# Performance work log

Hardware: AMD Instinct MI355X
Metric: run time of the kernel (lower is better)

Reference implementation:

```python
import jax, jax.numpy as jnp
import numpy as np

THRESHOLD = 0.5

def setup_inputs() -> dict:
    key = jax.random.key(0)
    k1, k2 = jax.random.split(key)
    N, F, B = 800000, 64, 8
    xs = jax.random.uniform(k1, (N, 1), dtype=jnp.float32)          # scores in [0,1)
    pl = jax.random.normal(k2, (N, F), dtype=jnp.float32)           # payload features
    rs = (jnp.arange(B + 1, dtype=jnp.int32) * (N // B))            # row splits [0,100k,...,800k]
    return {"xs": xs, "pl": pl, "rs": rs}

def reference(xs, pl, rs):
    # SelectThreshold(xs, pl, rs, threshold=0.5):
    #   keep rows with score > threshold, compact features, recompute row splits,
    #   and emit scatter indices (original row ids of the kept rows).
    # JIT-static variant: kept rows are stably compacted to the front of an
    # [N, F] buffer; slots >= n_sel are zero-padded, scatter idx padded with N.
    N = pl.shape[0]
    B = rs.shape[0] - 1
    mask = xs[:, 0] > THRESHOLD                                      # [N] bool
    # stable argsort: selected rows first, original (per-segment) order preserved
    order = jnp.argsort(jnp.logical_not(mask))                       # [N] int
    n_sel = jnp.sum(mask.astype(jnp.int32))
    valid = jnp.arange(N) < n_sel                                    # [N] bool
    newfeat = jnp.where(valid[:, None], pl[order], jnp.zeros((), pl.dtype))  # [N, F]
    scatter_idxs = jnp.where(valid, order, N).astype(jnp.int32)[:, None]     # [N, 1]
    # per-event selected counts -> new row splits
    seg_ids = jnp.searchsorted(rs, jnp.arange(N, dtype=rs.dtype), side='right') - 1  # [N]
    counts = jax.ops.segment_sum(mask.astype(rs.dtype), seg_ids, num_segments=B)     # [B]
    new_rs = jnp.concatenate([jnp.zeros((1,), rs.dtype), jnp.cumsum(counts)])        # [B+1]
    return newfeat, new_rs, scatter_idxs
```

## Files before the change

kernel.cpp:

```cpp
#include <hip/hip_runtime.h>


#define THRESH 0.5f
#define RPB 1024

__global__ void k_count(const float* __restrict__ xs, int N,
                        unsigned long long* __restrict__ bitmap,
                        int* __restrict__ blk_counts) {
    __shared__ int wc[16];
    const int tid  = threadIdx.x;
    const int lane = tid & 63, wave = tid >> 6;
    const int base = blockIdx.x * RPB;
    for (int c = 0; c < 4; ++c) {
        int i = base + c * 256 + tid;
        int m = (i < N) && (xs[i] > THRESH);
        unsigned long long bal = __ballot(m);
        if (lane == 0) {
            int rowstart = base + c * 256 + wave * 64;
            if (rowstart < N) bitmap[rowstart >> 6] = bal;
            wc[c * 4 + wave] = __popcll(bal);
        }
    }
    __syncthreads();
    if (tid == 0) {
        int s = 0;
        for (int k = 0; k < 16; ++k) s += wc[k];
        blk_counts[blockIdx.x] = s;
    }
}

__global__ void k_scan(const int* __restrict__ blk_counts, int nblocks,
                       const unsigned long long* __restrict__ bitmap,
                       const int* __restrict__ rs, int nrs, int N,
                       int* __restrict__ blk_off, int* __restrict__ nsel_out,
                       float* __restrict__ out_rs) {
    __shared__ int s[1024];
    const int t = threadIdx.x;
    int v = (t < nblocks) ? blk_counts[t] : 0;
    s[t] = v;
    __syncthreads();
    for (int d = 1; d < 1024; d <<= 1) {
        int add = (t >= d) ? s[t - d] : 0;
        __syncthreads();
        s[t] += add;
        __syncthreads();
    }
    int n_sel = s[1023];
    if (t < nblocks) blk_off[t] = s[t] - v;
    if (t == 0) nsel_out[0] = n_sel;
    if (t < nrs) {
        int j = rs[t];
        int val;
        if (j >= N)      val = n_sel;
        else if (j <= 0) val = 0;
        else {
            int blk = j >> 10;
            int cnt = (blk == 0) ? 0 : s[blk - 1];
            for (int w = (blk << 10) >> 6; w < (j >> 6); ++w)
                cnt += __popcll(bitmap[w]);
            int rem = j & 63;
            if (rem) cnt += __popcll(bitmap[j >> 6] & ((1ull << rem) - 1ull));
            val = cnt;
        }
        out_rs[t] = (float)val;
    }
}

__global__ void k_move(const float4* __restrict__ pl4,
                       const unsigned long long* __restrict__ bitmap,
                       const int* __restrict__ blk_off,
                       const int* __restrict__ nsel, int N, int nblocks,
                       float4* __restrict__ outf4, float* __restrict__ out_sc) {
    const int tid = threadIdx.x;
    const int b   = blockIdx.x;
    if (b < nblocks) {
        __shared__ unsigned long long w[16];
        __shared__ int wpre[16];
        __shared__ int rowid[RPB];
        const int base = b << 10;
        if (tid < 16) {
            int rowstart = base + (tid << 6);
            w[tid] = (rowstart < N) ? bitmap[(base >> 6) + tid] : 0ull;
        }
        __syncthreads();
        if (tid == 0) {
            int acc = 0;
            for (int k = 0; k < 16; ++k) { wpre[k] = acc; acc += __popcll(w[k]); }
        }
        __syncthreads();
        const int off = blk_off[b];
        for (int c = 0; c < 4; ++c) {
            int r = c * 256 + tid;
            int i = base + r;
            int k = r >> 6, bit = r & 63;
            unsigned long long bw = w[k];
            if (i < N && ((bw >> bit) & 1ull)) {
                int pre = wpre[k] + (int)__popcll(bw & ((1ull << bit) - 1ull));
                rowid[pre] = i;
                out_sc[off + pre] = (float)i;
            }
        }
        __syncthreads();
        const int cnt = wpre[15] + (int)__popcll(w[15]);
        const int cc  = tid & 15;
        for (int p = tid >> 4; p < cnt; p += 16) {
            int src = rowid[p];
            outf4[((size_t)(off + p)) * 16 + cc] = pl4[(size_t)src * 16 + cc];
        }
    } else {
        const int b2    = b - nblocks;
        const int start = b2 << 10;
        const int ns    = nsel[0];
        const int end   = min(start + RPB, N);
        if (end <= ns) return;
        const int lo = max(start, ns);
        for (int s = lo + tid; s < end; s += 256) out_sc[s] = (float)N;
        const int cc = tid & 15;
        const float4 z = make_float4(0.f, 0.f, 0.f, 0.f);
        for (int p = lo + (tid >> 4); p < end; p += 16)
            outf4[((size_t)p) * 16 + cc] = z;
    }
}

extern "C" void kernel_launch(void* const* d_in, const int* in_sizes, int n_in,
                              void* d_out, int out_size, void* d_ws, size_t ws_size,
                              hipStream_t stream) {
    const float* xs = (const float*)d_in[0];
    const float* pl = (const float*)d_in[1];
    const int*   rs = (const int*)d_in[2];
    const int N   = in_sizes[0];
    const int F   = in_sizes[1] / N;
    const int nrs = in_sizes[2];

    float* out      = (float*)d_out;
    float* out_feat = out;
    float* out_rs   = out + (size_t)N * F;
    float* out_sc   = out_rs + nrs;

    const int nwords = (N + 63) / 64;
    unsigned long long* bitmap = (unsigned long long*)d_ws;
    int* blk_counts = (int*)(bitmap + nwords);
    int* blk_off    = blk_counts + 1024;
    int* nsel       = blk_off + 1024;

    const int nblocks = (N + RPB - 1) / RPB;

    k_count<<<nblocks,     256,  0, stream>>>(xs, N, bitmap, blk_counts);
    k_scan <<<1,           1024, 0, stream>>>(blk_counts, nblocks, bitmap, rs, nrs, N,
                                              blk_off, nsel, out_rs);
    k_move <<<2 * nblocks, 256,  0, stream>>>((const float4*)pl, bitmap, blk_off, nsel,
                                              N, nblocks, (float4*)out_feat, out_sc);
}
```

Before: 366.2 us.

## Fuse count, scan and compaction into one decoupled-lookback kernel

Merges the three kernels (count, single-block scan, move) into one persistent-ticket kernel that uses a decoupled look-back prefix scan over per-block status words. Each block computes its mask, publishes an aggregate, looks back to get its offset, writes its compacted rows, row splits and scatter indices, then waits for the global total and zero-fills its share of the tail. This removes two kernel launches, the bitmap round trip through global memory and the second pass over the mask. In exchange it adds a memset, spin-waits on global atomics, and a serialising wait on the last block before the zero-fill.

```diff
diff --git a/kernel.cpp b/kernel.cpp
--- a/kernel.cpp
+++ b/kernel.cpp
@@ -4,122 +4,132 @@
 #define THRESH 0.5f
 #define RPB 1024
 
-__global__ void k_count(const float* __restrict__ xs, int N,
-                        unsigned long long* __restrict__ bitmap,
-                        int* __restrict__ blk_counts) {
-    __shared__ int wc[16];
+__global__ __launch_bounds__(256, 4)
+void k_all(const float* __restrict__ xs, const float4* __restrict__ pl4,
+           const int* __restrict__ rs, int nrs, int N, int nblocks,
+           int* __restrict__ ticket, unsigned* __restrict__ status,
+           float4* __restrict__ outf4, float* __restrict__ out_rs,
+           float* __restrict__ out_sc) {
+    __shared__ int s_t;
+    __shared__ unsigned long long w[16];
+    __shared__ int wpre[17];
+    __shared__ int s_off, s_nsel;
+    __shared__ int rowid[RPB];
+
     const int tid  = threadIdx.x;
     const int lane = tid & 63, wave = tid >> 6;
-    const int base = blockIdx.x * RPB;
+
+    if (tid == 0) s_t = atomicAdd(ticket, 1);
+    __syncthreads();
+    const int t    = s_t;
+    const int base = t << 10;
+    const int end  = min(base + RPB, N);
+
     for (int c = 0; c < 4; ++c) {
         int i = base + c * 256 + tid;
         int m = (i < N) && (xs[i] > THRESH);
         unsigned long long bal = __ballot(m);
+        if (lane == 0) w[c * 4 + wave] = bal;
+    }
+    __syncthreads();
+    if (tid == 0) {
+        int acc = 0;
+        for (int k = 0; k < 16; ++k) { wpre[k] = acc; acc += __popcll(w[k]); }
+        wpre[16] = acc;
+        unsigned flag = (t == 0) ? 2u : 1u;
+        __hip_atomic_store(&status[t], (flag << 30) | (unsigned)acc,
+                           __ATOMIC_RELEASE, __HIP_MEMORY_SCOPE_AGENT);
+    }
+    __syncthreads();
+    const int cnt = wpre[16];
+
+    if (wave == 0) {
+        int excl = 0;
+        if (t > 0) {
+            int idx = t - 1;
+            for (;;) {
+                int my = idx - lane;
+                unsigned st = 2u << 30;
+                bool done = (my < 0);
+                while (__ballot(!done)) {
+                    if (!done) {
+                        st = __hip_atomic_load(&status[my], __ATOMIC_ACQUIRE,
+                                               __HIP_MEMORY_SCOPE_AGENT);
+                        done = (st >> 30) != 0u;
+                    }
+                }
+                unsigned long long incl = __ballot((st >> 30) == 2u);
+                int firstIncl = (incl != 0ull) ? (__ffsll((unsigned long long)incl) - 1) : 64;
+                int val = (lane <= firstIncl) ? (int)(st & 0x3FFFFFFFu) : 0;
+                for (int o = 32; o > 0; o >>= 1) val += __shfl_down(val, o, 64);
+                excl += __shfl(val, 0, 64);
+                if (incl != 0ull) break;
+                idx -= 64;
+            }
+        }
         if (lane == 0) {
-            int rowstart = base + c * 256 + wave * 64;
-            if (rowstart < N) bitmap[rowstart >> 6] = bal;
-            wc[c * 4 + wave] = __popcll(bal);
+            s_off = excl;
+            __hip_atomic_store(&status[t], (2u << 30) | (unsigned)(excl + cnt),
+                               __ATOMIC_RELEASE, __HIP_MEMORY_SCOPE_AGENT);
         }
     }
     __syncthreads();
+    const int off = s_off;
+
+    for (int c = 0; c < 4; ++c) {
+        int r = c * 256 + tid;
+        int i = base + r;
+        int k = r >> 6, bit = r & 63;
+        unsigned long long bw = w[k];
+        if (i < N && ((bw >> bit) & 1ull)) {
+            int pre = wpre[k] + (int)__popcll(bw & ((1ull << bit) - 1ull));
+            rowid[pre] = i;
+            out_sc[off + pre] = (float)i;
+        }
+    }
+
+    if (tid < nrs) {
+        int j = rs[tid];
+        bool mine = (j == 0) ? (t == 0) : (j > base && j <= end);
+        if (mine) {
+            int val;
+            if (j == 0) val = 0;
+            else {
+                int d = j - base;
+                if (d == RPB) val = off + cnt;
+                else {
+                    int k = d >> 6, rem = d & 63;
+                    val = off + wpre[k] +
+                          (rem ? (int)__popcll(w[k] & ((1ull << rem) - 1ull)) : 0);
+                }
+            }
+            out_rs[tid] = (float)val;
+        }
+    }
+    __syncthreads();
+
+    const int cc = tid & 15;
+    for (int p = tid >> 4; p < cnt; p += 16) {
+        int src = rowid[p];
+        outf4[(size_t)(off + p) * 16 + cc] = pl4[(size_t)src * 16 + cc];
+    }
+
     if (tid == 0) {
-        int s = 0;
-        for (int k = 0; k < 16; ++k) s += wc[k];
-        blk_counts[blockIdx.x] = s;
+        unsigned st;
+        do {
+            st = __hip_atomic_load(&status[nblocks - 1], __ATOMIC_ACQUIRE,
+                                   __HIP_MEMORY_SCOPE_AGENT);
+        } while ((st >> 30) != 2u);
+        s_nsel = (int)(st & 0x3FFFFFFFu);
     }
-}
-
-__global__ void k_scan(const int* __restrict__ blk_counts, int nblocks,
-                       const unsigned long long* __restrict__ bitmap,
-                       const int* __restrict__ rs, int nrs, int N,
-                       int* __restrict__ blk_off, int* __restrict__ nsel_out,
-                       float* __restrict__ out_rs) {
-    __shared__ int s[1024];
-    const int t = threadIdx.x;
-    int v = (t < nblocks) ? blk_counts[t] : 0;
-    s[t] = v;
     __syncthreads();
-    for (int d = 1; d < 1024; d <<= 1) {
-        int add = (t >= d) ? s[t - d] : 0;
-        __syncthreads();
-        s[t] += add;
-        __syncthreads();
-    }
-    int n_sel = s[1023];
-    if (t < nblocks) blk_off[t] = s[t] - v;
-    if (t == 0) nsel_out[0] = n_sel;
-    if (t < nrs) {
-        int j = rs[t];
-        int val;
-        if (j >= N)      val = n_sel;
-        else if (j <= 0) val = 0;
-        else {
-            int blk = j >> 10;
-            int cnt = (blk == 0) ? 0 : s[blk - 1];
-            for (int w = (blk << 10) >> 6; w < (j >> 6); ++w)
-                cnt += __popcll(bitmap[w]);
-            int rem = j & 63;
-            if (rem) cnt += __popcll(bitmap[j >> 6] & ((1ull << rem) - 1ull));
-            val = cnt;
-        }
-        out_rs[t] = (float)val;
-    }
-}
-
-__global__ void k_move(const float4* __restrict__ pl4,
-                       const unsigned long long* __restrict__ bitmap,
-                       const int* __restrict__ blk_off,
-                       const int* __restrict__ nsel, int N, int nblocks,
-                       float4* __restrict__ outf4, float* __restrict__ out_sc) {
-    const int tid = threadIdx.x;
-    const int b   = blockIdx.x;
-    if (b < nblocks) {
-        __shared__ unsigned long long w[16];
-        __shared__ int wpre[16];
-        __shared__ int rowid[RPB];
-        const int base = b << 10;
-        if (tid < 16) {
-            int rowstart = base + (tid << 6);
-            w[tid] = (rowstart < N) ? bitmap[(base >> 6) + tid] : 0ull;
-        }
-        __syncthreads();
-        if (tid == 0) {
-            int acc = 0;
-            for (int k = 0; k < 16; ++k) { wpre[k] = acc; acc += __popcll(w[k]); }
-        }
-        __syncthreads();
-        const int off = blk_off[b];
-        for (int c = 0; c < 4; ++c) {
-            int r = c * 256 + tid;
-            int i = base + r;
-            int k = r >> 6, bit = r & 63;
-            unsigned long long bw = w[k];
-            if (i < N && ((bw >> bit) & 1ull)) {
-                int pre = wpre[k] + (int)__popcll(bw & ((1ull << bit) - 1ull));
-                rowid[pre] = i;
-                out_sc[off + pre] = (float)i;
-            }
-        }
-        __syncthreads();
-        const int cnt = wpre[15] + (int)__popcll(w[15]);
-        const int cc  = tid & 15;
-        for (int p = tid >> 4; p < cnt; p += 16) {
-            int src = rowid[p];
-            outf4[((size_t)(off + p)) * 16 + cc] = pl4[(size_t)src * 16 + cc];
-        }
-    } else {
-        const int b2    = b - nblocks;
-        const int start = b2 << 10;
-        const int ns    = nsel[0];
-        const int end   = min(start + RPB, N);
-        if (end <= ns) return;
-        const int lo = max(start, ns);
-        for (int s = lo + tid; s < end; s += 256) out_sc[s] = (float)N;
-        const int cc = tid & 15;
-        const float4 z = make_float4(0.f, 0.f, 0.f, 0.f);
-        for (int p = lo + (tid >> 4); p < end; p += 16)
-            outf4[((size_t)p) * 16 + cc] = z;
-    }
+    const int nsel  = s_nsel;
+    const int u_pre = base - off;
+    const int u     = (end - base) - cnt;
+    for (int p = tid; p < u; p += 256) out_sc[nsel + u_pre + p] = (float)N;
+    const float4 z = make_float4(0.f, 0.f, 0.f, 0.f);
+    for (int p = tid >> 4; p < u; p += 16)
+        outf4[(size_t)(nsel + u_pre + p) * 16 + cc] = z;
 }
 
 extern "C" void kernel_launch(void* const* d_in, const int* in_sizes, int n_in,
@@ -137,17 +147,14 @@
     float* out_rs   = out + (size_t)N * F;
     float* out_sc   = out_rs + nrs;
 
-    const int nwords = (N + 63) / 64;
-    unsigned long long* bitmap = (unsigned long long*)d_ws;
-    int* blk_counts = (int*)(bitmap + nwords);
-    int* blk_off    = blk_counts + 1024;
-    int* nsel       = blk_off + 1024;
+    int*      ticket = (int*)d_ws;
+    unsigned* status = (unsigned*)d_ws + 1;
 
     const int nblocks = (N + RPB - 1) / RPB;
 
-    k_count<<<nblocks,     256,  0, stream>>>(xs, N, bitmap, blk_counts);
-    k_scan <<<1,           1024, 0, stream>>>(blk_counts, nblocks, bitmap, rs, nrs, N,
-                                              blk_off, nsel, out_rs);
-    k_move <<<2 * nblocks, 256,  0, stream>>>((const float4*)pl, bitmap, blk_off, nsel,
-                                              N, nblocks, (float4*)out_feat, out_sc);
+    hipMemsetAsync(d_ws, 0, (size_t)(nblocks + 1) * sizeof(int), stream);
+
+    k_all<<<nblocks, 256, 0, stream>>>(xs, (const float4*)pl, rs, nrs, N, nblocks,
+                                       ticket, status, (float4*)out_feat,
+                                       out_rs, out_sc);
 }
```

New measurement: 442.5 us. 1.21x slower.
